# Kernel tuning notes

Measured on AMD Instinct MI355X. Metric: run time of the kernel, lower is better.

## Reference

```python
import jax, jax.numpy as jnp
import numpy as np

B, S, H = 2, 2048, 1024
NH = 16
HD = H // NH
SCALE = 1.0 / np.sqrt(HD).astype(np.float32)


def setup_inputs() -> dict:
    key = jax.random.key(0)
    ks = jax.random.split(key, 7)
    lim = 1.0 / np.sqrt(H)  # lecun-ish init scale for linear weights
    return {
        "query": jax.random.normal(ks[0], (B, S, H), dtype=jnp.float32),
        "key_in": jax.random.normal(ks[1], (B, S, H), dtype=jnp.float32),
        "value": jax.random.normal(ks[2], (B, S, H), dtype=jnp.float32),
        "attention_mask": jnp.ones((B, S), dtype=jnp.int32),
        "Wq": jax.random.uniform(ks[3], (H, H), jnp.float32, -lim, lim),
        "Wk": jax.random.uniform(ks[4], (H, H), jnp.float32, -lim, lim),
        "Wv": jax.random.uniform(ks[5], (H, H), jnp.float32, -lim, lim),
        "Wo": jax.random.uniform(ks[6], (H, H), jnp.float32, -lim, lim),
    }


def reference(query, key_in, value, attention_mask, Wq, Wk, Wv, Wo):
    b, s, _ = query.shape
    # projections (no bias)
    q = (query @ Wq).reshape(b, s, NH, HD).transpose(0, 2, 1, 3)  # [b,h,s,d]
    k = (key_in @ Wk).reshape(b, s, NH, HD).transpose(0, 2, 1, 3)
    v = (value @ Wv).reshape(b, s, NH, HD).transpose(0, 2, 1, 3)

    scores = jnp.einsum("bhqd,bhkd->bhqk", q, k) * SCALE  # [b,h,s,s]
    mask = attention_mask[:, None, None, :]  # broadcast over heads & query pos
    scores = jnp.where(mask == 0, -1e9, scores)
    attn = jax.nn.softmax(scores, axis=-1)

    ctx = jnp.einsum("bhqk,bhkd->bhqd", attn, v)
    ctx = ctx.transpose(0, 2, 1, 3).reshape(b, s, H)
    out = ctx @ Wo
    return out, jnp.mean(attn, axis=1)
```

## Files before the change

### kernel.cpp

```cpp
#include <hip/hip_runtime.h>
#include <stdint.h>

#define BB 2
#define SS 2048
#define HH 1024
#define NHEAD 16
#define HDIM 64

constexpr int   BSROWS = BB * SS;
constexpr float SCALE  = 0.125f;
constexpr float LOG2E  = 1.4426950408889634f;
constexpr float SL     = SCALE * LOG2E;

typedef __bf16 bf16;
typedef __attribute__((ext_vector_type(8))) __bf16 bf16x8;
typedef __attribute__((ext_vector_type(4))) __bf16 bf16x4;
typedef __attribute__((ext_vector_type(4))) float  f32x4;

#define MFMA16(a, b, c) __builtin_amdgcn_mfma_f32_16x16x32_bf16((a), (b), (c), 0, 0, 0)

__device__ __forceinline__ void gload_lds16(const void* g, void* l) {
  __builtin_amdgcn_global_load_lds((const __attribute__((address_space(1))) void*)g,
                                   (__attribute__((address_space(3))) void*)l, 16, 0, 0);
}

__global__ __launch_bounds__(256) void cvt_in(const float* __restrict__ q, const float* __restrict__ k,
                                              const float* __restrict__ v, const int* __restrict__ mask,
                                              bf16* __restrict__ xq, bf16* __restrict__ xk,
                                              bf16* __restrict__ xv, float* __restrict__ bias2) {
  int i = blockIdx.x * 256 + threadIdx.x;
  int e = i * 4;
  f32x4 a = *(const f32x4*)(q + e);
  f32x4 b = *(const f32x4*)(k + e);
  f32x4 c = *(const f32x4*)(v + e);
  *(bf16x4*)(xq + e) = __builtin_convertvector(a, bf16x4);
  *(bf16x4*)(xk + e) = __builtin_convertvector(b, bf16x4);
  *(bf16x4*)(xv + e) = __builtin_convertvector(c, bf16x4);
  if (i < BB * SS) bias2[i] = mask[i] ? 0.0f : -1e9f * LOG2E;
}

__global__ __launch_bounds__(256) void cvt_wt(const float* __restrict__ Wq, const float* __restrict__ Wk,
                                              const float* __restrict__ Wv, const float* __restrict__ Wo,
                                              bf16* __restrict__ Wt) {
  __shared__ float tile[32][33];
  int z = blockIdx.z;
  const float* W = (z == 0) ? Wq : (z == 1) ? Wk : (z == 2) ? Wv : Wo;
  bf16* out = Wt + (size_t)z * HH * HH;
  int bx = blockIdx.x * 32, by = blockIdx.y * 32;
  int tx = threadIdx.x, ty = threadIdx.y;
#pragma unroll
  for (int j = 0; j < 32; j += 8)
    tile[ty + j][tx] = W[(size_t)(by + ty + j) * HH + bx + tx];
  __syncthreads();
#pragma unroll
  for (int j = 0; j < 32; j += 8)
    out[(size_t)(bx + ty + j) * HH + by + tx] = (bf16)tile[tx][ty + j];
}

__global__ __launch_bounds__(256) void gemm128(const bf16* __restrict__ Abase, const bf16* __restrict__ Btbase,
                                               bf16* __restrict__ Qo, bf16* __restrict__ Ko,
                                               bf16* __restrict__ Vto, float* __restrict__ outF, int mode) {
  int zmode = (mode < 0) ? (int)blockIdx.z : mode;
  const bf16* A  = Abase  + (mode < 0 ? (size_t)blockIdx.z * BSROWS * HH : 0);
  const bf16* Bt = Btbase + (mode < 0 ? (size_t)blockIdx.z * HH * HH : 0);

  __shared__ __align__(16) bf16 lA[128 * 32];
  __shared__ __align__(16) bf16 lB[128 * 32];

  int t = threadIdx.x;
  int w = t >> 6, l = t & 63, lg = l >> 4, lr = l & 15;
  int m0 = blockIdx.y * 128, n0 = blockIdx.x * 128;
  int wr = (w >> 1) * 64, wc = (w & 1) * 64;

  f32x4 zero4 = {0.f, 0.f, 0.f, 0.f};
  f32x4 acc[4][4];
#pragma unroll
  for (int i = 0; i < 4; i++)
#pragma unroll
    for (int j = 0; j < 4; j++) acc[i][j] = zero4;

  for (int k0 = 0; k0 < HH; k0 += 32) {
#pragma unroll
    for (int i = 0; i < 2; i++) {
      int idx = i * 256 + t;
      gload_lds16(A  + (size_t)(m0 + (idx >> 2)) * HH + k0 + (idx & 3) * 8, &lA[(i * 256 + w * 64) * 8]);
      gload_lds16(Bt + (size_t)(n0 + (idx >> 2)) * HH + k0 + (idx & 3) * 8, &lB[(i * 256 + w * 64) * 8]);
    }
    __syncthreads();
    bf16x8 af[4], bq[4];
#pragma unroll
    for (int mi = 0; mi < 4; mi++) af[mi] = *(const bf16x8*)&lA[(wr + mi * 16 + lr) * 32 + lg * 8];
#pragma unroll
    for (int ni = 0; ni < 4; ni++) bq[ni] = *(const bf16x8*)&lB[(wc + ni * 16 + lr) * 32 + lg * 8];
#pragma unroll
    for (int mi = 0; mi < 4; mi++)
#pragma unroll
      for (int ni = 0; ni < 4; ni++)
        acc[mi][ni] = MFMA16(af[mi], bq[ni], acc[mi][ni]);
    __syncthreads();
  }

#pragma unroll
  for (int mi = 0; mi < 4; mi++) {
    int row0 = m0 + wr + mi * 16 + lg * 4;
#pragma unroll
    for (int ni = 0; ni < 4; ni++) {
      int col = n0 + wc + ni * 16 + lr;
      if (zmode == 3) {
#pragma unroll
        for (int r = 0; r < 4; r++) outF[(size_t)(row0 + r) * HH + col] = acc[mi][ni][r];
      } else if (zmode == 2) {
        int b = row0 >> 11, s0 = row0 & (SS - 1);
        int h = col >> 6, d = col & 63;
        bf16x4 pk;
#pragma unroll
        for (int r = 0; r < 4; r++) pk[r] = (bf16)acc[mi][ni][r];
        *(bf16x4*)&Vto[((size_t)(b * NHEAD + h) * HDIM + d) * SS + s0] = pk;
      } else {
        bf16* dst = (zmode == 0) ? Qo : Ko;
        int h = col >> 6, d = col & 63;
#pragma unroll
        for (int r = 0; r < 4; r++) {
          int row = row0 + r;
          int b = row >> 11, s = row & (SS - 1);
          dst[((size_t)(b * NHEAD + h) * SS + s) * HDIM + d] = (bf16)acc[mi][ni][r];
        }
      }
    }
  }
}

__global__ __launch_bounds__(256, 2) void attn_pv(const bf16* __restrict__ Q, const bf16* __restrict__ K,
                                                  const bf16* __restrict__ Vt, const float* __restrict__ bias2,
                                                  float* __restrict__ invl, bf16* __restrict__ ctx) {
  int b = blockIdx.z, h = blockIdx.y, q0 = blockIdx.x * 128;
  int t = threadIdx.x, w = t >> 6, l = t & 63, lg = l >> 4, lr = l & 15;
  size_t hb = ((size_t)b * NHEAD + h) * SS;
  const bf16* Qh = Q + hb * HDIM;
  const bf16* Kh = K + hb * HDIM;
  const bf16* Vh = Vt + ((size_t)b * NHEAD + h) * HDIM * SS;
  const float* biasb = bias2 + b * SS;

  __shared__ __align__(16) bf16 sK[64][72];
  __shared__ __align__(16) bf16 sV[64][72];
  __shared__ __align__(16) bf16 lp[4][32][72];

  int r0 = t >> 3, c0 = (t & 7) * 8;
  bf16x8 kreg[2], vreg[2];

  int qa = q0 + w * 32;
  int rowa = qa + lr, rowb = qa + 16 + lr;
  bf16x8 qf0a = *(const bf16x8*)&Qh[(size_t)rowa * HDIM + lg * 8];
  bf16x8 qf1a = *(const bf16x8*)&Qh[(size_t)rowa * HDIM + 32 + lg * 8];
  bf16x8 qf0b = *(const bf16x8*)&Qh[(size_t)rowb * HDIM + lg * 8];
  bf16x8 qf1b = *(const bf16x8*)&Qh[(size_t)rowb * HDIM + 32 + lg * 8];

  f32x4 zero4 = {0.f, 0.f, 0.f, 0.f};
  f32x4 lacca = zero4, laccb = zero4;
  f32x4 ctxa[4], ctxb[4];
#pragma unroll
  for (int nd = 0; nd < 4; nd++) { ctxa[nd] = zero4; ctxb[nd] = zero4; }

#pragma unroll
  for (int i = 0; i < 2; i++) {
    int row = i * 32 + r0;
    kreg[i] = *(const bf16x8*)&Kh[(size_t)row * HDIM + c0];
    vreg[i] = *(const bf16x8*)&Vh[(size_t)row * SS + c0];
  }
#pragma unroll
  for (int i = 0; i < 2; i++) {
    int row = i * 32 + r0;
    *(bf16x8*)&sK[row][c0] = kreg[i];
    *(bf16x8*)&sV[row][c0] = vreg[i];
  }

  for (int kt = 0; kt < 32; kt++) {
    int k0 = kt * 64;
    __syncthreads();
    if (kt < 31) {
      int kn = k0 + 64;
#pragma unroll
      for (int i = 0; i < 2; i++) {
        int row = i * 32 + r0;
        kreg[i] = *(const bf16x8*)&Kh[(size_t)(kn + row) * HDIM + c0];
        vreg[i] = *(const bf16x8*)&Vh[(size_t)row * SS + kn + c0];
      }
    }
    f32x4 acca[4], accb[4];
#pragma unroll
    for (int ni = 0; ni < 4; ni++) {
      const bf16* kp = &sK[ni * 16 + lr][lg * 8];
      bf16x8 kf0 = *(const bf16x8*)kp;
      bf16x8 kf1 = *(const bf16x8*)(kp + 32);
      acca[ni] = MFMA16(kf1, qf1a, MFMA16(kf0, qf0a, zero4));
      accb[ni] = MFMA16(kf1, qf1b, MFMA16(kf0, qf0b, zero4));
    }
    f32x4 pa4[4], pb4[4];
#pragma unroll
    for (int ni = 0; ni < 4; ni++) {
      f32x4 bv = *(const f32x4*)&biasb[k0 + ni * 16 + lg * 4];
      f32x4 za = acca[ni] * SL + bv;
      f32x4 zb = accb[ni] * SL + bv;
#pragma unroll
      for (int r = 0; r < 4; r++) {
        pa4[ni][r] = __builtin_amdgcn_exp2f(za[r]);
        pb4[ni][r] = __builtin_amdgcn_exp2f(zb[r]);
      }
    }
    lacca += (pa4[0] + pa4[1]) + (pa4[2] + pa4[3]);
    laccb += (pb4[0] + pb4[1]) + (pb4[2] + pb4[3]);
#pragma unroll
    for (int ni = 0; ni < 4; ni++) {
      *(bf16x4*)&lp[w][lr][ni * 16 + lg * 4]      = __builtin_convertvector(pa4[ni], bf16x4);
      *(bf16x4*)&lp[w][16 + lr][ni * 16 + lg * 4] = __builtin_convertvector(pb4[ni], bf16x4);
    }
#pragma unroll
    for (int kk = 0; kk < 2; kk++) {
      bf16x8 paa = *(const bf16x8*)&lp[w][lr][kk * 32 + lg * 8];
      bf16x8 pab = *(const bf16x8*)&lp[w][16 + lr][kk * 32 + lg * 8];
#pragma unroll
      for (int nd = 0; nd < 4; nd++) {
        bf16x8 vf = *(const bf16x8*)&sV[nd * 16 + lr][kk * 32 + lg * 8];
        ctxa[nd] = MFMA16(paa, vf, ctxa[nd]);
        ctxb[nd] = MFMA16(pab, vf, ctxb[nd]);
      }
    }
    __syncthreads();
    if (kt < 31) {
#pragma unroll
      for (int i = 0; i < 2; i++) {
        int row = i * 32 + r0;
        *(bf16x8*)&sK[row][c0] = kreg[i];
        *(bf16x8*)&sV[row][c0] = vreg[i];
      }
    }
  }

  float lsa = (lacca[0] + lacca[1]) + (lacca[2] + lacca[3]);
  float lsb = (laccb[0] + laccb[1]) + (laccb[2] + laccb[3]);
  lsa += __shfl_xor(lsa, 16); lsa += __shfl_xor(lsa, 32);
  lsb += __shfl_xor(lsb, 16); lsb += __shfl_xor(lsb, 32);
  float ila = 1.0f / lsa, ilb = 1.0f / lsb;
  f32x4 ilva, ilvb;
#pragma unroll
  for (int r = 0; r < 4; r++) { ilva[r] = __shfl(ila, lg * 4 + r); ilvb[r] = __shfl(ilb, lg * 4 + r); }
#pragma unroll
  for (int nd = 0; nd < 4; nd++)
#pragma unroll
    for (int r = 0; r < 4; r++) {
      int ra = qa + lg * 4 + r, rb = qa + 16 + lg * 4 + r;
      ctx[(size_t)(b * SS + ra) * HH + h * HDIM + nd * 16 + lr] = (bf16)(ctxa[nd][r] * ilva[r]);
      ctx[(size_t)(b * SS + rb) * HH + h * HDIM + nd * 16 + lr] = (bf16)(ctxb[nd][r] * ilvb[r]);
    }
  if (l < 16) {
    invl[hb + qa + l]      = ila;
    invl[hb + qa + 16 + l] = ilb;
  }
}

__global__ __launch_bounds__(256, 4) void attn_mean(const bf16* __restrict__ Q, const bf16* __restrict__ K,
                                                    const float* __restrict__ bias2,
                                                    const float* __restrict__ invl, float* __restrict__ meanOut) {
  int q0 = blockIdx.x * 128, kc0 = blockIdx.y * 64, b = blockIdx.z;
  int t = threadIdx.x, w = t >> 6, l = t & 63, lg = l >> 4, lr = l & 15;
  const float* biasb = bias2 + b * SS;
  __shared__ __align__(16) bf16 sK[2][64][72];

  int qa = q0 + w * 32;
  int rowa = qa + lr, rowb = qa + 16 + lr;
  int sr = t >> 3, sc = (t & 7) * 8;

  f32x4 bv[4];
#pragma unroll
  for (int ni = 0; ni < 4; ni++) bv[ni] = *(const f32x4*)&biasb[kc0 + ni * 16 + lg * 4];

  f32x4 zero4 = {0.f, 0.f, 0.f, 0.f};
  f32x4 macca[4], maccb[4];
#pragma unroll
  for (int ni = 0; ni < 4; ni++) { macca[ni] = zero4; maccb[ni] = zero4; }

  bf16x8 kreg0, kreg1, qf0a, qf1a, qf0b, qf1b;
  float ila, ilb;
  {
    const bf16* Kh0 = K + ((size_t)b * NHEAD) * SS * HDIM;
    kreg0 = *(const bf16x8*)&Kh0[(size_t)(kc0 + sr) * HDIM + sc];
    kreg1 = *(const bf16x8*)&Kh0[(size_t)(kc0 + sr + 32) * HDIM + sc];
    const bf16* Qh0 = Q + ((size_t)b * NHEAD) * SS * HDIM;
    qf0a = *(const bf16x8*)&Qh0[(size_t)rowa * HDIM + lg * 8];
    qf1a = *(const bf16x8*)&Qh0[(size_t)rowa * HDIM + 32 + lg * 8];
    qf0b = *(const bf16x8*)&Qh0[(size_t)rowb * HDIM + lg * 8];
    qf1b = *(const bf16x8*)&Qh0[(size_t)rowb * HDIM + 32 + lg * 8];
    size_t hb0 = (size_t)b * NHEAD * SS;
    ila = invl[hb0 + rowa] * (1.0f / NHEAD);
    ilb = invl[hb0 + rowb] * (1.0f / NHEAD);
    *(bf16x8*)&sK[0][sr][sc]      = kreg0;
    *(bf16x8*)&sK[0][sr + 32][sc] = kreg1;
  }
  __syncthreads();

  for (int h = 0; h < NHEAD; h++) {
    int cur = h & 1;
    bf16x8 qn0a, qn1a, qn0b, qn1b;
    float ina = 0.f, inb = 0.f;
    if (h < NHEAD - 1) {
      size_t hbn = ((size_t)b * NHEAD + h + 1) * SS;
      const bf16* Khn = K + hbn * HDIM;
      kreg0 = *(const bf16x8*)&Khn[(size_t)(kc0 + sr) * HDIM + sc];
      kreg1 = *(const bf16x8*)&Khn[(size_t)(kc0 + sr + 32) * HDIM + sc];
      const bf16* Qhn = Q + hbn * HDIM;
      qn0a = *(const bf16x8*)&Qhn[(size_t)rowa * HDIM + lg * 8];
      qn1a = *(const bf16x8*)&Qhn[(size_t)rowa * HDIM + 32 + lg * 8];
      qn0b = *(const bf16x8*)&Qhn[(size_t)rowb * HDIM + lg * 8];
      qn1b = *(const bf16x8*)&Qhn[(size_t)rowb * HDIM + 32 + lg * 8];
      ina = invl[hbn + rowa] * (1.0f / NHEAD);
      inb = invl[hbn + rowb] * (1.0f / NHEAD);
    }
#pragma unroll
    for (int ni = 0; ni < 4; ni++) {
      const bf16* kp = &sK[cur][ni * 16 + lr][lg * 8];
      bf16x8 kf0 = *(const bf16x8*)kp;
      bf16x8 kf1 = *(const bf16x8*)(kp + 32);
      f32x4 acca = MFMA16(kf1, qf1a, MFMA16(kf0, qf0a, zero4));
      f32x4 accb = MFMA16(kf1, qf1b, MFMA16(kf0, qf0b, zero4));
      f32x4 za = acca * SL + bv[ni];
      f32x4 zb = accb * SL + bv[ni];
#pragma unroll
      for (int r = 0; r < 4; r++) {
        macca[ni][r] += __builtin_amdgcn_exp2f(za[r]) * ila;
        maccb[ni][r] += __builtin_amdgcn_exp2f(zb[r]) * ilb;
      }
    }
    if (h < NHEAD - 1) {
      *(bf16x8*)&sK[cur ^ 1][sr][sc]      = kreg0;
      *(bf16x8*)&sK[cur ^ 1][sr + 32][sc] = kreg1;
      qf0a = qn0a; qf1a = qn1a; qf0b = qn0b; qf1b = qn1b;
      ila = ina; ilb = inb;
      __syncthreads();
    }
  }
  float* meanB = meanOut + (size_t)b * SS * SS;
#pragma unroll
  for (int ni = 0; ni < 4; ni++) {
    *(f32x4*)&meanB[(size_t)rowa * SS + kc0 + ni * 16 + lg * 4] = macca[ni];
    *(f32x4*)&meanB[(size_t)rowb * SS + kc0 + ni * 16 + lg * 4] = maccb[ni];
  }
}

extern "C" void kernel_launch(void* const* d_in, const int* in_sizes, int n_in,
                              void* d_out, int out_size, void* d_ws, size_t ws_size,
                              hipStream_t stream) {
  const float* query  = (const float*)d_in[0];
  const float* key_in = (const float*)d_in[1];
  const float* value  = (const float*)d_in[2];
  const int*   mask   = (const int*)d_in[3];
  const float* Wq     = (const float*)d_in[4];
  const float* Wk     = (const float*)d_in[5];
  const float* Wv     = (const float*)d_in[6];
  const float* Wo     = (const float*)d_in[7];

  char* ws = (char*)d_ws;
  bf16*  Xb    = (bf16*)(ws);
  bf16*  Wt    = (bf16*)(ws + 25165824);
  bf16*  Qb    = (bf16*)(ws + 33554432);
  bf16*  Kb    = (bf16*)(ws + 41943040);
  bf16*  Vtb   = (bf16*)(ws + 50331648);
  float* invlb = (float*)(ws + 58982400);
  float* biasb = (float*)(ws + 59244544);
  bf16*  ctxb  = Xb;

  float* outF  = (float*)d_out;
  float* meanF = outF + (size_t)BB * SS * HH;

  cvt_in<<<4096, 256, 0, stream>>>(query, key_in, value, mask,
                                   Xb, Xb + 4194304, Xb + 8388608, biasb);
  cvt_wt<<<dim3(32, 32, 4), dim3(32, 8), 0, stream>>>(Wq, Wk, Wv, Wo, Wt);
  gemm128<<<dim3(8, 32, 3), 256, 0, stream>>>(Xb, Wt, Qb, Kb, Vtb, nullptr, -1);
  attn_pv<<<dim3(16, 16, 2), 256, 0, stream>>>(Qb, Kb, Vtb, biasb, invlb, ctxb);
  attn_mean<<<dim3(16, 32, 2), 256, 0, stream>>>(Qb, Kb, biasb, invlb, meanF);
  gemm128<<<dim3(8, 32, 1), 256, 0, stream>>>(ctxb, Wt + 3 * (size_t)HH * HH,
                                              nullptr, nullptr, nullptr, outF, 3);
}
```

Before: 204.6 us.

## Use direct global-to-LDS loads with XOR swizzle and double buffering in attention kernels

The attention PV and mean-attention kernels now load K/V tiles with global_load_lds straight into XOR-swizzled, double-buffered LDS instead of staging them through registers into padded arrays. This drops a barrier per iteration in attn_pv and frees registers, while the swizzle avoids bank conflicts without padding. The GEMM also remaps block IDs so that neighbouring workgroups spread across XCDs, for better L2 locality. The risk is that the async LDS loads are not properly waited on before the barrier, and that the block remap assumes fixed grid dimensions.

```diff
diff --git a/kernel.cpp b/kernel.cpp
--- a/kernel.cpp
+++ b/kernel.cpp
@@ -60,16 +60,21 @@
 __global__ __launch_bounds__(256) void gemm128(const bf16* __restrict__ Abase, const bf16* __restrict__ Btbase,
                                                bf16* __restrict__ Qo, bf16* __restrict__ Ko,
                                                bf16* __restrict__ Vto, float* __restrict__ outF, int mode) {
-  int zmode = (mode < 0) ? (int)blockIdx.z : mode;
-  const bf16* A  = Abase  + (mode < 0 ? (size_t)blockIdx.z * BSROWS * HH : 0);
-  const bf16* Bt = Btbase + (mode < 0 ? (size_t)blockIdx.z * HH * HH : 0);
+  int id  = blockIdx.x + 8 * blockIdx.y + 256 * blockIdx.z;
+  int nwg = 256 * gridDim.z;
+  int sw  = (id & 7) * (nwg >> 3) + (id >> 3);
+  int bx  = sw & 7, by = (sw >> 3) & 31, bz = sw >> 8;
+
+  int zmode = (mode < 0) ? bz : mode;
+  const bf16* A  = Abase  + (mode < 0 ? (size_t)bz * BSROWS * HH : 0);
+  const bf16* Bt = Btbase + (mode < 0 ? (size_t)bz * HH * HH : 0);
 
   __shared__ __align__(16) bf16 lA[128 * 32];
   __shared__ __align__(16) bf16 lB[128 * 32];
 
   int t = threadIdx.x;
   int w = t >> 6, l = t & 63, lg = l >> 4, lr = l & 15;
-  int m0 = blockIdx.y * 128, n0 = blockIdx.x * 128;
+  int m0 = by * 128, n0 = bx * 128;
   int wr = (w >> 1) * 64, wc = (w & 1) * 64;
 
   f32x4 zero4 = {0.f, 0.f, 0.f, 0.f};
@@ -141,12 +146,13 @@
   const bf16* Vh = Vt + ((size_t)b * NHEAD + h) * HDIM * SS;
   const float* biasb = bias2 + b * SS;
 
-  __shared__ __align__(16) bf16 sK[64][72];
-  __shared__ __align__(16) bf16 sV[64][72];
+  __shared__ __align__(16) bf16 sK[2][64][64];
+  __shared__ __align__(16) bf16 sV[2][64][64];
   __shared__ __align__(16) bf16 lp[4][32][72];
 
-  int r0 = t >> 3, c0 = (t & 7) * 8;
-  bf16x8 kreg[2], vreg[2];
+  int rloc = l >> 3;
+  int csw  = (l & 7) ^ (rloc & 7);
+  int swz  = lr & 7;
 
   int qa = q0 + w * 32;
   int rowa = qa + lr, rowb = qa + 16 + lr;
@@ -163,35 +169,28 @@
 
 #pragma unroll
   for (int i = 0; i < 2; i++) {
-    int row = i * 32 + r0;
-    kreg[i] = *(const bf16x8*)&Kh[(size_t)row * HDIM + c0];
-    vreg[i] = *(const bf16x8*)&Vh[(size_t)row * SS + c0];
-  }
-#pragma unroll
-  for (int i = 0; i < 2; i++) {
-    int row = i * 32 + r0;
-    *(bf16x8*)&sK[row][c0] = kreg[i];
-    *(bf16x8*)&sV[row][c0] = vreg[i];
-  }
+    int rs = w * 16 + i * 8;
+    gload_lds16(Kh + (size_t)(rs + rloc) * HDIM + csw * 8, &sK[0][rs][0]);
+    gload_lds16(Vh + (size_t)(rs + rloc) * SS + csw * 8,   &sV[0][rs][0]);
+  }
+  __syncthreads();
 
   for (int kt = 0; kt < 32; kt++) {
-    int k0 = kt * 64;
-    __syncthreads();
+    int k0 = kt * 64, cur = kt & 1;
     if (kt < 31) {
       int kn = k0 + 64;
 #pragma unroll
       for (int i = 0; i < 2; i++) {
-        int row = i * 32 + r0;
-        kreg[i] = *(const bf16x8*)&Kh[(size_t)(kn + row) * HDIM + c0];
-        vreg[i] = *(const bf16x8*)&Vh[(size_t)row * SS + kn + c0];
+        int rs = w * 16 + i * 8;
+        gload_lds16(Kh + (size_t)(kn + rs + rloc) * HDIM + csw * 8, &sK[cur ^ 1][rs][0]);
+        gload_lds16(Vh + (size_t)(rs + rloc) * SS + kn + csw * 8,   &sV[cur ^ 1][rs][0]);
       }
     }
     f32x4 acca[4], accb[4];
 #pragma unroll
     for (int ni = 0; ni < 4; ni++) {
-      const bf16* kp = &sK[ni * 16 + lr][lg * 8];
-      bf16x8 kf0 = *(const bf16x8*)kp;
-      bf16x8 kf1 = *(const bf16x8*)(kp + 32);
+      bf16x8 kf0 = *(const bf16x8*)&sK[cur][ni * 16 + lr][(lg ^ swz) * 8];
+      bf16x8 kf1 = *(const bf16x8*)&sK[cur][ni * 16 + lr][((4 + lg) ^ swz) * 8];
       acca[ni] = MFMA16(kf1, qf1a, MFMA16(kf0, qf0a, zero4));
       accb[ni] = MFMA16(kf1, qf1b, MFMA16(kf0, qf0b, zero4));
     }
@@ -220,20 +219,12 @@
       bf16x8 pab = *(const bf16x8*)&lp[w][16 + lr][kk * 32 + lg * 8];
 #pragma unroll
       for (int nd = 0; nd < 4; nd++) {
-        bf16x8 vf = *(const bf16x8*)&sV[nd * 16 + lr][kk * 32 + lg * 8];
+        bf16x8 vf = *(const bf16x8*)&sV[cur][nd * 16 + lr][((kk * 4 + lg) ^ swz) * 8];
         ctxa[nd] = MFMA16(paa, vf, ctxa[nd]);
         ctxb[nd] = MFMA16(pab, vf, ctxb[nd]);
       }
     }
-    __syncthreads();
-    if (kt < 31) {
-#pragma unroll
-      for (int i = 0; i < 2; i++) {
-        int row = i * 32 + r0;
-        *(bf16x8*)&sK[row][c0] = kreg[i];
-        *(bf16x8*)&sV[row][c0] = vreg[i];
-      }
-    }
+    if (kt < 31) __syncthreads();
   }
 
   float lsa = (lacca[0] + lacca[1]) + (lacca[2] + lacca[3]);
@@ -264,11 +255,14 @@
   int q0 = blockIdx.x * 128, kc0 = blockIdx.y * 64, b = blockIdx.z;
   int t = threadIdx.x, w = t >> 6, l = t & 63, lg = l >> 4, lr = l & 15;
   const float* biasb = bias2 + b * SS;
-  __shared__ __align__(16) bf16 sK[2][64][72];
+  __shared__ __align__(16) bf16 sK[2][64][64];
+
+  int rloc = l >> 3;
+  int csw  = (l & 7) ^ (rloc & 7);
+  int swz  = lr & 7;
 
   int qa = q0 + w * 32;
   int rowa = qa + lr, rowb = qa + 16 + lr;
-  int sr = t >> 3, sc = (t & 7) * 8;
 
   f32x4 bv[4];
 #pragma unroll
@@ -279,12 +273,15 @@
 #pragma unroll
   for (int ni = 0; ni < 4; ni++) { macca[ni] = zero4; maccb[ni] = zero4; }
 
-  bf16x8 kreg0, kreg1, qf0a, qf1a, qf0b, qf1b;
+  bf16x8 qf0a, qf1a, qf0b, qf1b;
   float ila, ilb;
   {
     const bf16* Kh0 = K + ((size_t)b * NHEAD) * SS * HDIM;
-    kreg0 = *(const bf16x8*)&Kh0[(size_t)(kc0 + sr) * HDIM + sc];
-    kreg1 = *(const bf16x8*)&Kh0[(size_t)(kc0 + sr + 32) * HDIM + sc];
+#pragma unroll
+    for (int i = 0; i < 2; i++) {
+      int rs = w * 16 + i * 8;
+      gload_lds16(Kh0 + (size_t)(kc0 + rs + rloc) * HDIM + csw * 8, &sK[0][rs][0]);
+    }
     const bf16* Qh0 = Q + ((size_t)b * NHEAD) * SS * HDIM;
     qf0a = *(const bf16x8*)&Qh0[(size_t)rowa * HDIM + lg * 8];
     qf1a = *(const bf16x8*)&Qh0[(size_t)rowa * HDIM + 32 + lg * 8];
@@ -293,8 +290,6 @@
     size_t hb0 = (size_t)b * NHEAD * SS;
     ila = invl[hb0 + rowa] * (1.0f / NHEAD);
     ilb = invl[hb0 + rowb] * (1.0f / NHEAD);
-    *(bf16x8*)&sK[0][sr][sc]      = kreg0;
-    *(bf16x8*)&sK[0][sr + 32][sc] = kreg1;
   }
   __syncthreads();
 
@@ -305,8 +300,11 @@
     if (h < NHEAD - 1) {
       size_t hbn = ((size_t)b * NHEAD + h + 1) * SS;
       const bf16* Khn = K + hbn * HDIM;
-      kreg0 = *(const bf16x8*)&Khn[(size_t)(kc0 + sr) * HDIM + sc];
-      kreg1 = *(const bf16x8*)&Khn[(size_t)(kc0 + sr + 32) * HDIM + sc];
+#pragma unroll
+      for (int i = 0; i < 2; i++) {
+        int rs = w * 16 + i * 8;
+        gload_lds16(Khn + (size_t)(kc0 + rs + rloc) * HDIM + csw * 8, &sK[cur ^ 1][rs][0]);
+      }
       const bf16* Qhn = Q + hbn * HDIM;
       qn0a = *(const bf16x8*)&Qhn[(size_t)rowa * HDIM + lg * 8];
       qn1a = *(const bf16x8*)&Qhn[(size_t)rowa * HDIM + 32 + lg * 8];
@@ -317,9 +315,8 @@
     }
 #pragma unroll
     for (int ni = 0; ni < 4; ni++) {
-      const bf16* kp = &sK[cur][ni * 16 + lr][lg * 8];
-      bf16x8 kf0 = *(const bf16x8*)kp;
-      bf16x8 kf1 = *(const bf16x8*)(kp + 32);
+      bf16x8 kf0 = *(const bf16x8*)&sK[cur][ni * 16 + lr][(lg ^ swz) * 8];
+      bf16x8 kf1 = *(const bf16x8*)&sK[cur][ni * 16 + lr][((4 + lg) ^ swz) * 8];
       f32x4 acca = MFMA16(kf1, qf1a, MFMA16(kf0, qf0a, zero4));
       f32x4 accb = MFMA16(kf1, qf1b, MFMA16(kf0, qf0b, zero4));
       f32x4 za = acca * SL + bv[ni];
@@ -331,8 +328,6 @@
       }
     }
     if (h < NHEAD - 1) {
-      *(bf16x8*)&sK[cur ^ 1][sr][sc]      = kreg0;
-      *(bf16x8*)&sK[cur ^ 1][sr + 32][sc] = kreg1;
       qf0a = qn0a; qf1a = qn1a; qf0b = qn0b; qf1b = qn1b;
       ila = ina; ilb = inb;
       __syncthreads();
```

Result: slower. 210.1 us (+2.7%).

## Remap workgroup IDs across XCDs and load attn_mean K tiles directly to LDS

Applied to the files above, without the earlier changes.

Block indices in gemm128, attn_pv and attn_mean are remapped so that consecutive workgroups, which are dispatched round-robin across the eight XCDs, work on neighbouring tiles, aiming to improve L2 locality per XCD. In attn_mean, K tiles are now loaded with global_load_lds straight into an unpadded, XOR-swizzled LDS buffer instead of being staged through registers. This drops the register round-trip and the padding, while the swizzle is meant to avoid bank conflicts. The risk is that the remap assumes fixed grid dimensions, and the async LDS loads need correct synchronisation before the double buffer is reused.

```diff
diff --git a/kernel.cpp b/kernel.cpp
--- a/kernel.cpp
+++ b/kernel.cpp
@@ -60,16 +60,21 @@
 __global__ __launch_bounds__(256) void gemm128(const bf16* __restrict__ Abase, const bf16* __restrict__ Btbase,
                                                bf16* __restrict__ Qo, bf16* __restrict__ Ko,
                                                bf16* __restrict__ Vto, float* __restrict__ outF, int mode) {
-  int zmode = (mode < 0) ? (int)blockIdx.z : mode;
-  const bf16* A  = Abase  + (mode < 0 ? (size_t)blockIdx.z * BSROWS * HH : 0);
-  const bf16* Bt = Btbase + (mode < 0 ? (size_t)blockIdx.z * HH * HH : 0);
+  int id  = blockIdx.x + 8 * blockIdx.y + 256 * blockIdx.z;
+  int nwg = 256 * gridDim.z;
+  int sw  = (id & 7) * (nwg >> 3) + (id >> 3);
+  int bx  = sw & 7, by = (sw >> 3) & 31, bz = sw >> 8;
+
+  int zmode = (mode < 0) ? bz : mode;
+  const bf16* A  = Abase  + (mode < 0 ? (size_t)bz * BSROWS * HH : 0);
+  const bf16* Bt = Btbase + (mode < 0 ? (size_t)bz * HH * HH : 0);
 
   __shared__ __align__(16) bf16 lA[128 * 32];
   __shared__ __align__(16) bf16 lB[128 * 32];
 
   int t = threadIdx.x;
   int w = t >> 6, l = t & 63, lg = l >> 4, lr = l & 15;
-  int m0 = blockIdx.y * 128, n0 = blockIdx.x * 128;
+  int m0 = by * 128, n0 = bx * 128;
   int wr = (w >> 1) * 64, wc = (w & 1) * 64;
 
   f32x4 zero4 = {0.f, 0.f, 0.f, 0.f};
@@ -133,7 +138,9 @@
 __global__ __launch_bounds__(256, 2) void attn_pv(const bf16* __restrict__ Q, const bf16* __restrict__ K,
                                                   const bf16* __restrict__ Vt, const float* __restrict__ bias2,
                                                   float* __restrict__ invl, bf16* __restrict__ ctx) {
-  int b = blockIdx.z, h = blockIdx.y, q0 = blockIdx.x * 128;
+  int id = blockIdx.x + 16 * blockIdx.y + 256 * blockIdx.z;
+  int sw = (id & 7) * 64 + (id >> 3);
+  int b = sw >> 8, h = (sw >> 4) & 15, q0 = (sw & 15) * 128;
   int t = threadIdx.x, w = t >> 6, l = t & 63, lg = l >> 4, lr = l & 15;
   size_t hb = ((size_t)b * NHEAD + h) * SS;
   const bf16* Qh = Q + hb * HDIM;
@@ -261,14 +268,19 @@
 __global__ __launch_bounds__(256, 4) void attn_mean(const bf16* __restrict__ Q, const bf16* __restrict__ K,
                                                     const float* __restrict__ bias2,
                                                     const float* __restrict__ invl, float* __restrict__ meanOut) {
-  int q0 = blockIdx.x * 128, kc0 = blockIdx.y * 64, b = blockIdx.z;
+  int id = blockIdx.x + 16 * blockIdx.y + 512 * blockIdx.z;
+  int sw = (id & 7) * 128 + (id >> 3);
+  int b = sw >> 9, kc0 = ((sw >> 4) & 31) * 64, q0 = (sw & 15) * 128;
   int t = threadIdx.x, w = t >> 6, l = t & 63, lg = l >> 4, lr = l & 15;
   const float* biasb = bias2 + b * SS;
-  __shared__ __align__(16) bf16 sK[2][64][72];
+  __shared__ __align__(16) bf16 sK[2][64][64];
+
+  int rloc = l >> 3;
+  int csw  = (l & 7) ^ (rloc & 7);
+  int swz  = lr & 7;
 
   int qa = q0 + w * 32;
   int rowa = qa + lr, rowb = qa + 16 + lr;
-  int sr = t >> 3, sc = (t & 7) * 8;
 
   f32x4 bv[4];
 #pragma unroll
@@ -279,12 +291,15 @@
 #pragma unroll
   for (int ni = 0; ni < 4; ni++) { macca[ni] = zero4; maccb[ni] = zero4; }
 
-  bf16x8 kreg0, kreg1, qf0a, qf1a, qf0b, qf1b;
+  bf16x8 qf0a, qf1a, qf0b, qf1b;
   float ila, ilb;
   {
     const bf16* Kh0 = K + ((size_t)b * NHEAD) * SS * HDIM;
-    kreg0 = *(const bf16x8*)&Kh0[(size_t)(kc0 + sr) * HDIM + sc];
-    kreg1 = *(const bf16x8*)&Kh0[(size_t)(kc0 + sr + 32) * HDIM + sc];
+#pragma unroll
+    for (int i = 0; i < 2; i++) {
+      int rs = w * 16 + i * 8;
+      gload_lds16(Kh0 + (size_t)(kc0 + rs + rloc) * HDIM + csw * 8, &sK[0][rs][0]);
+    }
     const bf16* Qh0 = Q + ((size_t)b * NHEAD) * SS * HDIM;
     qf0a = *(const bf16x8*)&Qh0[(size_t)rowa * HDIM + lg * 8];
     qf1a = *(const bf16x8*)&Qh0[(size_t)rowa * HDIM + 32 + lg * 8];
@@ -293,8 +308,6 @@
     size_t hb0 = (size_t)b * NHEAD * SS;
     ila = invl[hb0 + rowa] * (1.0f / NHEAD);
     ilb = invl[hb0 + rowb] * (1.0f / NHEAD);
-    *(bf16x8*)&sK[0][sr][sc]      = kreg0;
-    *(bf16x8*)&sK[0][sr + 32][sc] = kreg1;
   }
   __syncthreads();
 
@@ -305,8 +318,11 @@
     if (h < NHEAD - 1) {
       size_t hbn = ((size_t)b * NHEAD + h + 1) * SS;
       const bf16* Khn = K + hbn * HDIM;
-      kreg0 = *(const bf16x8*)&Khn[(size_t)(kc0 + sr) * HDIM + sc];
-      kreg1 = *(const bf16x8*)&Khn[(size_t)(kc0 + sr + 32) * HDIM + sc];
+#pragma unroll
+      for (int i = 0; i < 2; i++) {
+        int rs = w * 16 + i * 8;
+        gload_lds16(Khn + (size_t)(kc0 + rs + rloc) * HDIM + csw * 8, &sK[cur ^ 1][rs][0]);
+      }
       const bf16* Qhn = Q + hbn * HDIM;
       qn0a = *(const bf16x8*)&Qhn[(size_t)rowa * HDIM + lg * 8];
       qn1a = *(const bf16x8*)&Qhn[(size_t)rowa * HDIM + 32 + lg * 8];
@@ -317,9 +333,8 @@
     }
 #pragma unroll
     for (int ni = 0; ni < 4; ni++) {
-      const bf16* kp = &sK[cur][ni * 16 + lr][lg * 8];
-      bf16x8 kf0 = *(const bf16x8*)kp;
-      bf16x8 kf1 = *(const bf16x8*)(kp + 32);
+      bf16x8 kf0 = *(const bf16x8*)&sK[cur][ni * 16 + lr][(lg ^ swz) * 8];
+      bf16x8 kf1 = *(const bf16x8*)&sK[cur][ni * 16 + lr][((4 + lg) ^ swz) * 8];
       f32x4 acca = MFMA16(kf1, qf1a, MFMA16(kf0, qf0a, zero4));
       f32x4 accb = MFMA16(kf1, qf1b, MFMA16(kf0, qf0b, zero4));
       f32x4 za = acca * SL + bv[ni];
@@ -331,8 +346,6 @@
       }
     }
     if (h < NHEAD - 1) {
-      *(bf16x8*)&sK[cur ^ 1][sr][sc]      = kreg0;
-      *(bf16x8*)&sK[cur ^ 1][sr + 32][sc] = kreg1;
       qf0a = qn0a; qf1a = qn1a; qf0b = qn0b; qf1b = qn1b;
       ila = ina; ilb = inb;
       __syncthreads();
```

New measurement: 192.5 us. 1.06x faster.
